# Kernel tuning notes

Hardware: AMD Instinct MI355X
Metric: run time of the kernel (lower is better)

## Reference

```python
import jax, jax.numpy as jnp
import numpy as np

DECAY = 0.8
EPS = 1e-05


def setup_inputs() -> dict:
    key = jax.random.key(0)
    k1, k2, k3 = jax.random.split(key, 3)
    x = jax.random.normal(k1, (8, 2048, 256), dtype=jnp.float32)
    embed = jax.random.normal(k2, (8192, 256), dtype=jnp.float32)
    cluster_size = jnp.zeros((8192,), dtype=jnp.float32)
    embed_avg = jax.random.normal(k3, (8192, 256), dtype=jnp.float32)
    return {"x": x, "embed": embed, "cluster_size": cluster_size, "embed_avg": embed_avg}


def reference(x, embed, cluster_size, embed_avg):
    codebook_size, dim = embed.shape
    shape = x.shape
    flatten = x.reshape(-1, dim)  # [N, d]

    dist = -(jnp.sum(flatten ** 2, axis=1, keepdims=True)
             - 2.0 * flatten @ embed.T
             + jnp.sum(embed ** 2, axis=1)[None, :])  # [N, C]
    embed_ind_flat = jnp.argmax(dist, axis=-1)  # [N]
    embed_ind = embed_ind_flat.reshape(shape[:-1])
    quantize = jnp.take(embed, embed_ind_flat, axis=0).reshape(shape)

    # EMA update (training branch). onehot matmuls expressed as segment sums.
    counts = jax.ops.segment_sum(jnp.ones_like(embed_ind_flat, dtype=x.dtype),
                                 embed_ind_flat, num_segments=codebook_size)  # [C]
    embed_sum = jax.ops.segment_sum(flatten, embed_ind_flat,
                                    num_segments=codebook_size)  # [C, d]
    cluster_size_new = cluster_size * DECAY + (1.0 - DECAY) * counts
    embed_avg_new = embed_avg * DECAY + (1.0 - DECAY) * embed_sum
    smoothed = (cluster_size_new + EPS) / (cluster_size_new.sum() + codebook_size * EPS)
    cs = smoothed * cluster_size_new.sum()
    embed_normalized = embed_avg_new / cs[:, None]

    return quantize, embed_ind, embed_normalized, cluster_size_new, embed_avg_new
```

## Files before the change

kernel.cpp:

```cpp
#include <hip/hip_runtime.h>
#include <hip/hip_bf16.h>

#define DECAY_F 0.8f
#define OMD_F   0.2f
#define EPS_F   1e-5f

#define NROWS 16384
#define CBOOK 8192
#define DIM   256
#define KSPLIT 768

#define WS_KEYS   0u
#define WS_ENORM  131072u
#define WS_COUNTS 163840u
#define WS_TOTAL  196608u
#define WS_XSPLIT 262144u
#define WS_ESPLIT 25428008u
#define WS_ESPLIT_OFF (262144u + 25165824u)
#define WS_NEED   (WS_ESPLIT_OFF + 12582912u)

#define O_QUANT 0
#define O_IND   4194304
#define O_NORM  4210688
#define O_CSN   6307840
#define O_AVG   6316032

typedef __attribute__((ext_vector_type(8))) short short8;
typedef __attribute__((ext_vector_type(4))) float f32x4;
typedef __attribute__((ext_vector_type(4))) unsigned short us4;

__device__ __forceinline__ unsigned int fkey(float f) {
    unsigned int b = __float_as_uint(f);
    return (b & 0x80000000u) ? ~b : (b | 0x80000000u);
}
__device__ __forceinline__ unsigned short f2bf(float f) {
    unsigned int u = __float_as_uint(f);
    unsigned int r = (u + 0x7FFFu + ((u >> 16) & 1u)) >> 16;
    return (unsigned short)r;
}
__device__ __forceinline__ float bf2f(unsigned short h) {
    return __uint_as_float(((unsigned int)h) << 16);
}

#define GLOAD_LDS16(g, l) \
    __builtin_amdgcn_global_load_lds((const __attribute__((address_space(1))) void*)(g), \
                                     (__attribute__((address_space(3))) void*)(l), 16, 0, 0)

__global__ __launch_bounds__(256) void enorm_kernel(const float* __restrict__ embed,
                                                    float* __restrict__ enorm) {
    int row  = (blockIdx.x * 256 + threadIdx.x) >> 6;
    int lane = threadIdx.x & 63;
    float4 v = *(const float4*)&embed[row * DIM + lane * 4];
    float s = v.x * v.x + v.y * v.y + v.z * v.z + v.w * v.w;
    for (int m = 32; m >= 1; m >>= 1) s += __shfl_xor(s, m, 64);
    if (lane == 0) enorm[row] = s;
}

__global__ __launch_bounds__(256) void init_avg_kernel(const float* __restrict__ embed_avg,
                                                       float* __restrict__ avg_out) {
    int i = blockIdx.x * 256 + threadIdx.x;
    float4 v = ((const float4*)embed_avg)[i];
    v.x *= DECAY_F; v.y *= DECAY_F; v.z *= DECAY_F; v.w *= DECAY_F;
    ((float4*)avg_out)[i] = v;
}

__global__ __launch_bounds__(256) void split_kernel(const float* __restrict__ src,
                                                    unsigned short* __restrict__ dst,
                                                    int pat) {
    int i = blockIdx.x * 256 + threadIdx.x;
    int e4  = i * 4;
    int row = e4 >> 8;
    int k   = e4 & 255;
    float4 v = ((const float4*)src)[i];
    us4 hi, lo;
    hi.x = f2bf(v.x); lo.x = f2bf(v.x - bf2f(hi.x));
    hi.y = f2bf(v.y); lo.y = f2bf(v.y - bf2f(hi.y));
    hi.z = f2bf(v.z); lo.z = f2bf(v.z - bf2f(hi.z));
    hi.w = f2bf(v.w); lo.w = f2bf(v.w - bf2f(hi.w));
    unsigned short* base = dst + (size_t)row * KSPLIT + k;
    *(us4*)(base + 0)   = hi;
    if (pat == 0) {
        *(us4*)(base + 256) = lo;
        *(us4*)(base + 512) = hi;
    } else {
        *(us4*)(base + 256) = hi;
        *(us4*)(base + 512) = lo;
    }
}

__global__ __launch_bounds__(256) void mfma_argmin_kernel(const unsigned short* __restrict__ A,
                                                          const unsigned short* __restrict__ B,
                                                          const float* __restrict__ enorm,
                                                          unsigned long long* __restrict__ keys) {
    __shared__ __align__(16) unsigned short Al[128 * 32];
    __shared__ __align__(16) unsigned short Bl[128 * 32];

    const int tid  = threadIdx.x;
    const int lane = tid & 63;
    const int wid  = tid >> 6;
    const int wr = wid >> 1, wc = wid & 1;
    const int mBase = blockIdx.y * 128;
    const int nBase = blockIdx.x * 128;

    const int lr = lane & 15;
    const int lk = (lane >> 4) * 8;

    f32x4 acc[4][4];
#pragma unroll
    for (int i = 0; i < 4; i++)
#pragma unroll
        for (int n = 0; n < 4; n++) acc[i][n] = (f32x4)0.f;

    const int r0  = tid >> 2;
    const int ck0 = (tid & 3) * 8;
    const unsigned short* srcA0 = A + (size_t)(mBase + r0) * KSPLIT + ck0;
    const unsigned short* srcA1 = srcA0 + (size_t)64 * KSPLIT;
    const unsigned short* srcB0 = B + (size_t)(nBase + r0) * KSPLIT + ck0;
    const unsigned short* srcB1 = srcB0 + (size_t)64 * KSPLIT;
    unsigned short* dstA0 = Al + tid * 8;
    unsigned short* dstA1 = Al + (tid + 256) * 8;
    unsigned short* dstB0 = Bl + tid * 8;
    unsigned short* dstB1 = Bl + (tid + 256) * 8;

    for (int kk = 0; kk < KSPLIT; kk += 32) {
        __syncthreads();
        GLOAD_LDS16(srcA0 + kk, dstA0);
        GLOAD_LDS16(srcA1 + kk, dstA1);
        GLOAD_LDS16(srcB0 + kk, dstB0);
        GLOAD_LDS16(srcB1 + kk, dstB1);
        __syncthreads();

        short8 af[4], bf[4];
#pragma unroll
        for (int i = 0; i < 4; i++)
            af[i] = *(const short8*)&Al[(wr * 64 + i * 16 + lr) * 32 + lk];
#pragma unroll
        for (int n = 0; n < 4; n++)
            bf[n] = *(const short8*)&Bl[(wc * 64 + n * 16 + lr) * 32 + lk];
#pragma unroll
        for (int i = 0; i < 4; i++)
#pragma unroll
            for (int n = 0; n < 4; n++)
                acc[i][n] = __builtin_amdgcn_mfma_f32_16x16x32_bf16(af[i], bf[n], acc[i][n], 0, 0, 0);
    }

    float en4[4];
    int   c4[4];
#pragma unroll
    for (int n = 0; n < 4; n++) {
        c4[n]  = nBase + wc * 64 + n * 16 + lr;
        en4[n] = enorm[c4[n]];
    }
#pragma unroll
    for (int i = 0; i < 4; i++) {
#pragma unroll
        for (int reg = 0; reg < 4; reg++) {
            float bs = 3.4e38f; int bc = 0;
#pragma unroll
            for (int n = 0; n < 4; n++) {
                float s = en4[n] - 2.f * acc[i][n][reg];
                if (s < bs || (s == bs && c4[n] < bc)) { bs = s; bc = c4[n]; }
            }
            unsigned long long key =
                ((unsigned long long)fkey(bs) << 32) | (unsigned int)bc;
#pragma unroll
            for (int m = 8; m >= 1; m >>= 1) {
                unsigned long long o = __shfl_xor(key, m, 64);
                if (o < key) key = o;
            }
            if (lr == 0)
                atomicMin(&keys[mBase + wr * 64 + i * 16 + (lane >> 4) * 4 + reg], key);
        }
    }
}

#define BM 64
#define BN 256
#define KB 16
#define NSPLIT 4

__global__ __launch_bounds__(256) void argmin_kernel(const float* __restrict__ x,
                                                     const float* __restrict__ embed,
                                                     const float* __restrict__ enorm,
                                                     unsigned long long* __restrict__ keys) {
    __shared__ float xs[KB][BM];
    __shared__ float es[KB][BN];

    const int tid = threadIdx.x;
    const int tx = tid & 31;
    const int ty = tid >> 5;
    const int rowBase = blockIdx.x * BM;
    const int cStart = blockIdx.y * (CBOOK / NSPLIT);

    float bestS[8];
    int   bestC[8];
#pragma unroll
    for (int i = 0; i < 8; i++) { bestS[i] = 3.4e38f; bestC[i] = 0; }

    float acc[8][8];

    for (int cb = 0; cb < CBOOK / NSPLIT; cb += BN) {
        const int cbase = cStart + cb;
#pragma unroll
        for (int i = 0; i < 8; i++)
#pragma unroll
            for (int j = 0; j < 8; j++) acc[i][j] = 0.f;

        for (int kk = 0; kk < DIM; kk += KB) {
            __syncthreads();
            {
                int r  = tid >> 2;
                int k4 = (tid & 3) * 4;
                float4 v = *(const float4*)&x[(rowBase + r) * DIM + kk + k4];
                xs[k4 + 0][r] = v.x; xs[k4 + 1][r] = v.y;
                xs[k4 + 2][r] = v.z; xs[k4 + 3][r] = v.w;
            }
            {
                const float4* src = (const float4*)&embed[(cbase + tid) * DIM + kk];
#pragma unroll
                for (int q = 0; q < 4; q++) {
                    float4 v = src[q];
                    es[q * 4 + 0][tid] = v.x; es[q * 4 + 1][tid] = v.y;
                    es[q * 4 + 2][tid] = v.z; es[q * 4 + 3][tid] = v.w;
                }
            }
            __syncthreads();
#pragma unroll
            for (int k = 0; k < KB; k++) {
                float xr[8], er[8];
                *(float4*)&xr[0] = *(const float4*)&xs[k][ty * 8];
                *(float4*)&xr[4] = *(const float4*)&xs[k][ty * 8 + 4];
                *(float4*)&er[0] = *(const float4*)&es[k][tx * 4];
                *(float4*)&er[4] = *(const float4*)&es[k][128 + tx * 4];
#pragma unroll
                for (int i = 0; i < 8; i++)
#pragma unroll
                    for (int j = 0; j < 8; j++)
                        acc[i][j] = fmaf(xr[i], er[j], acc[i][j]);
            }
        }
#pragma unroll
        for (int j = 0; j < 8; j++) {
            int c = cbase + ((j < 4) ? (tx * 4 + j) : (128 + tx * 4 + (j - 4)));
            float en = enorm[c];
#pragma unroll
            for (int i = 0; i < 8; i++) {
                float s = en - 2.f * acc[i][j];
                if (s < bestS[i]) { bestS[i] = s; bestC[i] = c; }
            }
        }
    }

#pragma unroll
    for (int i = 0; i < 8; i++) {
        unsigned long long key =
            ((unsigned long long)fkey(bestS[i]) << 32) | (unsigned int)bestC[i];
        for (int m = 16; m >= 1; m >>= 1) {
            unsigned long long o = __shfl_xor(key, m, 64);
            if (o < key) key = o;
        }
        if (tx == 0) atomicMin(&keys[rowBase + ty * 8 + i], key);
    }
}

__global__ __launch_bounds__(256) void scatter_kernel(const float* __restrict__ x,
                                                      const float* __restrict__ embed,
                                                      const unsigned long long* __restrict__ keys,
                                                      float* __restrict__ quant,
                                                      float* __restrict__ ind_out,
                                                      float* __restrict__ counts,
                                                      float* __restrict__ avg_out) {
    int i = blockIdx.x * 256 + threadIdx.x;
    int row = i >> 6;
    int c4  = (i & 63) * 4;
    int idx = (int)(keys[row] & 0xFFFFFFFFull);
    float4 e = *(const float4*)&embed[idx * DIM + c4];
    *(float4*)&quant[row * DIM + c4] = e;
    float4 xv = *(const float4*)&x[row * DIM + c4];
    atomicAdd(&avg_out[idx * DIM + c4 + 0], OMD_F * xv.x);
    atomicAdd(&avg_out[idx * DIM + c4 + 1], OMD_F * xv.y);
    atomicAdd(&avg_out[idx * DIM + c4 + 2], OMD_F * xv.z);
    atomicAdd(&avg_out[idx * DIM + c4 + 3], OMD_F * xv.w);
    if ((i & 63) == 0) {
        ind_out[row] = (float)idx;
        atomicAdd(&counts[idx], 1.0f);
    }
}

__global__ __launch_bounds__(256) void csn_kernel(const float* __restrict__ cluster_size,
                                                  const float* __restrict__ counts,
                                                  float* __restrict__ csn_out,
                                                  float* __restrict__ total) {
    int c = blockIdx.x * 256 + threadIdx.x;
    float v = DECAY_F * cluster_size[c] + OMD_F * counts[c];
    csn_out[c] = v;
    float s = v;
    for (int m = 32; m >= 1; m >>= 1) s += __shfl_xor(s, m, 64);
    __shared__ float ws4[4];
    if ((threadIdx.x & 63) == 0) ws4[threadIdx.x >> 6] = s;
    __syncthreads();
    if (threadIdx.x == 0) atomicAdd(total, ws4[0] + ws4[1] + ws4[2] + ws4[3]);
}

__global__ __launch_bounds__(256) void norm_kernel(const float* __restrict__ avg_new,
                                                   const float* __restrict__ csn,
                                                   const float* __restrict__ total,
                                                   float* __restrict__ out) {
    int i = blockIdx.x * 256 + threadIdx.x;
    int c = i >> 6;
    float tot = *total;
    float smoothed = (csn[c] + EPS_F) / (tot + (float)CBOOK * EPS_F);
    float cs = smoothed * tot;
    float4 v = ((const float4*)avg_new)[i];
    v.x = v.x / cs; v.y = v.y / cs; v.z = v.z / cs; v.w = v.w / cs;
    ((float4*)out)[i] = v;
}

extern "C" void kernel_launch(void* const* d_in, const int* in_sizes, int n_in,
                              void* d_out, int out_size, void* d_ws, size_t ws_size,
                              hipStream_t stream) {
    const float* x            = (const float*)d_in[0];
    const float* embed        = (const float*)d_in[1];
    const float* cluster_size = (const float*)d_in[2];
    const float* embed_avg    = (const float*)d_in[3];
    float* out = (float*)d_out;
    char*  ws  = (char*)d_ws;

    unsigned long long* keys = (unsigned long long*)(ws + WS_KEYS);
    float* enorm  = (float*)(ws + WS_ENORM);
    float* counts = (float*)(ws + WS_COUNTS);
    float* total  = (float*)(ws + WS_TOTAL);

    hipMemsetAsync(ws + WS_KEYS, 0xFF, NROWS * 8, stream);
    hipMemsetAsync(ws + WS_COUNTS, 0, CBOOK * 4 + 4, stream);

    enorm_kernel<<<CBOOK / 4, 256, 0, stream>>>(embed, enorm);
    init_avg_kernel<<<(CBOOK * DIM / 4) / 256, 256, 0, stream>>>(embed_avg, out + O_AVG);

    if (ws_size >= (size_t)WS_NEED) {
        unsigned short* xsplit = (unsigned short*)(ws + WS_XSPLIT);
        unsigned short* esplit = (unsigned short*)(ws + WS_ESPLIT_OFF);
        split_kernel<<<(NROWS * DIM / 4) / 256, 256, 0, stream>>>(x, xsplit, 0);
        split_kernel<<<(CBOOK * DIM / 4) / 256, 256, 0, stream>>>(embed, esplit, 1);
        dim3 grid(CBOOK / 128, NROWS / 128);
        mfma_argmin_kernel<<<grid, 256, 0, stream>>>(xsplit, esplit, enorm, keys);
    } else {
        dim3 grid(NROWS / BM, NSPLIT);
        argmin_kernel<<<grid, 256, 0, stream>>>(x, embed, enorm, keys);
    }

    scatter_kernel<<<(NROWS * DIM / 4) / 256, 256, 0, stream>>>(
        x, embed, keys, out + O_QUANT, out + O_IND, counts, out + O_AVG);

    csn_kernel<<<CBOOK / 256, 256, 0, stream>>>(cluster_size, counts, out + O_CSN, total);

    norm_kernel<<<(CBOOK * DIM / 4) / 256, 256, 0, stream>>>(
        out + O_AVG, out + O_CSN, total, out + O_NORM);
}
```

Baseline: 454.4 us.

## Double-buffer LDS with swizzle in MFMA argmin and fuse enorm into esplit

The MFMA distance kernel now double-buffers its LDS tiles, so the global-to-LDS loads for the next K slice are issued before the current slice's MFMAs, with one barrier per iteration instead of two. It also XOR-swizzles the 16-byte chunk layout in LDS to cut bank conflicts on fragment reads, and adds an occupancy hint to launch bounds. Separately, the codebook norm computation is folded into the embed split kernel, which removes one launch and one read of the codebook. The trade-off is twice the LDS per block, which may limit occupancy.

```diff
diff --git a/kernel.cpp b/kernel.cpp
--- a/kernel.cpp
+++ b/kernel.cpp
@@ -15,7 +15,6 @@
 #define WS_COUNTS 163840u
 #define WS_TOTAL  196608u
 #define WS_XSPLIT 262144u
-#define WS_ESPLIT 25428008u
 #define WS_ESPLIT_OFF (262144u + 25165824u)
 #define WS_NEED   (WS_ESPLIT_OFF + 12582912u)
 
@@ -45,16 +44,6 @@
 #define GLOAD_LDS16(g, l) \
     __builtin_amdgcn_global_load_lds((const __attribute__((address_space(1))) void*)(g), \
                                      (__attribute__((address_space(3))) void*)(l), 16, 0, 0)
-
-__global__ __launch_bounds__(256) void enorm_kernel(const float* __restrict__ embed,
-                                                    float* __restrict__ enorm) {
-    int row  = (blockIdx.x * 256 + threadIdx.x) >> 6;
-    int lane = threadIdx.x & 63;
-    float4 v = *(const float4*)&embed[row * DIM + lane * 4];
-    float s = v.x * v.x + v.y * v.y + v.z * v.z + v.w * v.w;
-    for (int m = 32; m >= 1; m >>= 1) s += __shfl_xor(s, m, 64);
-    if (lane == 0) enorm[row] = s;
-}
 
 __global__ __launch_bounds__(256) void init_avg_kernel(const float* __restrict__ embed_avg,
                                                        float* __restrict__ avg_out) {
@@ -64,9 +53,8 @@
     ((float4*)avg_out)[i] = v;
 }
 
-__global__ __launch_bounds__(256) void split_kernel(const float* __restrict__ src,
-                                                    unsigned short* __restrict__ dst,
-                                                    int pat) {
+__global__ __launch_bounds__(256) void xsplit_kernel(const float* __restrict__ src,
+                                                     unsigned short* __restrict__ dst) {
     int i = blockIdx.x * 256 + threadIdx.x;
     int e4  = i * 4;
     int row = e4 >> 8;
@@ -79,21 +67,36 @@
     hi.w = f2bf(v.w); lo.w = f2bf(v.w - bf2f(hi.w));
     unsigned short* base = dst + (size_t)row * KSPLIT + k;
     *(us4*)(base + 0)   = hi;
-    if (pat == 0) {
-        *(us4*)(base + 256) = lo;
-        *(us4*)(base + 512) = hi;
-    } else {
-        *(us4*)(base + 256) = hi;
-        *(us4*)(base + 512) = lo;
-    }
-}
-
-__global__ __launch_bounds__(256) void mfma_argmin_kernel(const unsigned short* __restrict__ A,
-                                                          const unsigned short* __restrict__ B,
-                                                          const float* __restrict__ enorm,
-                                                          unsigned long long* __restrict__ keys) {
-    __shared__ __align__(16) unsigned short Al[128 * 32];
-    __shared__ __align__(16) unsigned short Bl[128 * 32];
+    *(us4*)(base + 256) = lo;
+    *(us4*)(base + 512) = hi;
+}
+
+__global__ __launch_bounds__(256) void esplit_kernel(const float* __restrict__ embed,
+                                                     unsigned short* __restrict__ dst,
+                                                     float* __restrict__ enorm) {
+    int row  = (blockIdx.x * 256 + threadIdx.x) >> 6;
+    int lane = threadIdx.x & 63;
+    float4 v = *(const float4*)&embed[row * DIM + lane * 4];
+    float s = v.x * v.x + v.y * v.y + v.z * v.z + v.w * v.w;
+    for (int m = 32; m >= 1; m >>= 1) s += __shfl_xor(s, m, 64);
+    if (lane == 0) enorm[row] = s;
+    us4 hi, lo;
+    hi.x = f2bf(v.x); lo.x = f2bf(v.x - bf2f(hi.x));
+    hi.y = f2bf(v.y); lo.y = f2bf(v.y - bf2f(hi.y));
+    hi.z = f2bf(v.z); lo.z = f2bf(v.z - bf2f(hi.z));
+    hi.w = f2bf(v.w); lo.w = f2bf(v.w - bf2f(hi.w));
+    unsigned short* base = dst + (size_t)row * KSPLIT + lane * 4;
+    *(us4*)(base + 0)   = hi;
+    *(us4*)(base + 256) = hi;
+    *(us4*)(base + 512) = lo;
+}
+
+__global__ __launch_bounds__(256, 4) void mfma_argmin_kernel(const unsigned short* __restrict__ A,
+                                                             const unsigned short* __restrict__ B,
+                                                             const float* __restrict__ enorm,
+                                                             unsigned long long* __restrict__ keys) {
+    __shared__ __align__(16) unsigned short Al[2][128 * 32];
+    __shared__ __align__(16) unsigned short Bl[2][128 * 32];
 
     const int tid  = threadIdx.x;
     const int lane = tid & 63;
@@ -103,7 +106,7 @@
     const int nBase = blockIdx.x * 128;
 
     const int lr = lane & 15;
-    const int lk = (lane >> 4) * 8;
+    const int hk = lane >> 4;
 
     f32x4 acc[4][4];
 #pragma unroll
@@ -111,38 +114,50 @@
 #pragma unroll
         for (int n = 0; n < 4; n++) acc[i][n] = (f32x4)0.f;
 
-    const int r0  = tid >> 2;
-    const int ck0 = (tid & 3) * 8;
-    const unsigned short* srcA0 = A + (size_t)(mBase + r0) * KSPLIT + ck0;
-    const unsigned short* srcA1 = srcA0 + (size_t)64 * KSPLIT;
-    const unsigned short* srcB0 = B + (size_t)(nBase + r0) * KSPLIT + ck0;
-    const unsigned short* srcB1 = srcB0 + (size_t)64 * KSPLIT;
-    unsigned short* dstA0 = Al + tid * 8;
-    unsigned short* dstA1 = Al + (tid + 256) * 8;
-    unsigned short* dstB0 = Bl + tid * 8;
-    unsigned short* dstB1 = Bl + (tid + 256) * 8;
-
-    for (int kk = 0; kk < KSPLIT; kk += 32) {
+    const int r0 = tid >> 2;
+    const int ck = (((tid & 3) ^ ((r0 >> 1) & 3)) << 3);
+    const unsigned short* gA0 = A + (size_t)(mBase + r0) * KSPLIT + ck;
+    const unsigned short* gA1 = gA0 + (size_t)64 * KSPLIT;
+    const unsigned short* gB0 = B + (size_t)(nBase + r0) * KSPLIT + ck;
+    const unsigned short* gB1 = gB0 + (size_t)64 * KSPLIT;
+
+#define STAGE(b, kk) do { \
+    GLOAD_LDS16(gA0 + (kk), &Al[b][tid * 8]); \
+    GLOAD_LDS16(gA1 + (kk), &Al[b][(tid + 256) * 8]); \
+    GLOAD_LDS16(gB0 + (kk), &Bl[b][tid * 8]); \
+    GLOAD_LDS16(gB1 + (kk), &Bl[b][(tid + 256) * 8]); \
+} while (0)
+
+    const int co = ((hk ^ ((lr >> 1) & 3)) << 3);
+    int aoff[4], boff[4];
+#pragma unroll
+    for (int i = 0; i < 4; i++) {
+        aoff[i] = (wr * 64 + i * 16 + lr) * 32 + co;
+        boff[i] = (wc * 64 + i * 16 + lr) * 32 + co;
+    }
+
+    STAGE(0, 0);
+    __syncthreads();
+
+#pragma unroll 2
+    for (int t = 0; t < 24; ++t) {
+        const int cur = t & 1;
+        if (t < 23) STAGE(cur ^ 1, (t + 1) * 32);
+
+        short8 af[4], bf4[4];
+#pragma unroll
+        for (int i = 0; i < 4; i++) af[i]  = *(const short8*)&Al[cur][aoff[i]];
+#pragma unroll
+        for (int n = 0; n < 4; n++) bf4[n] = *(const short8*)&Bl[cur][boff[n]];
+#pragma unroll
+        for (int i = 0; i < 4; i++)
+#pragma unroll
+            for (int n = 0; n < 4; n++)
+                acc[i][n] = __builtin_amdgcn_mfma_f32_16x16x32_bf16(af[i], bf4[n], acc[i][n], 0, 0, 0);
+
         __syncthreads();
-        GLOAD_LDS16(srcA0 + kk, dstA0);
-        GLOAD_LDS16(srcA1 + kk, dstA1);
-        GLOAD_LDS16(srcB0 + kk, dstB0);
-        GLOAD_LDS16(srcB1 + kk, dstB1);
-        __syncthreads();
-
-        short8 af[4], bf[4];
-#pragma unroll
-        for (int i = 0; i < 4; i++)
-            af[i] = *(const short8*)&Al[(wr * 64 + i * 16 + lr) * 32 + lk];
-#pragma unroll
-        for (int n = 0; n < 4; n++)
-            bf[n] = *(const short8*)&Bl[(wc * 64 + n * 16 + lr) * 32 + lk];
-#pragma unroll
-        for (int i = 0; i < 4; i++)
-#pragma unroll
-            for (int n = 0; n < 4; n++)
-                acc[i][n] = __builtin_amdgcn_mfma_f32_16x16x32_bf16(af[i], bf[n], acc[i][n], 0, 0, 0);
-    }
+    }
+#undef STAGE
 
     float en4[4];
     int   c4[4];
@@ -169,7 +184,7 @@
                 if (o < key) key = o;
             }
             if (lr == 0)
-                atomicMin(&keys[mBase + wr * 64 + i * 16 + (lane >> 4) * 4 + reg], key);
+                atomicMin(&keys[mBase + wr * 64 + i * 16 + hk * 4 + reg], key);
         }
     }
 }
@@ -334,17 +349,17 @@
     hipMemsetAsync(ws + WS_KEYS, 0xFF, NROWS * 8, stream);
     hipMemsetAsync(ws + WS_COUNTS, 0, CBOOK * 4 + 4, stream);
 
-    enorm_kernel<<<CBOOK / 4, 256, 0, stream>>>(embed, enorm);
     init_avg_kernel<<<(CBOOK * DIM / 4) / 256, 256, 0, stream>>>(embed_avg, out + O_AVG);
 
     if (ws_size >= (size_t)WS_NEED) {
         unsigned short* xsplit = (unsigned short*)(ws + WS_XSPLIT);
         unsigned short* esplit = (unsigned short*)(ws + WS_ESPLIT_OFF);
-        split_kernel<<<(NROWS * DIM / 4) / 256, 256, 0, stream>>>(x, xsplit, 0);
-        split_kernel<<<(CBOOK * DIM / 4) / 256, 256, 0, stream>>>(embed, esplit, 1);
+        xsplit_kernel<<<(NROWS * DIM / 4) / 256, 256, 0, stream>>>(x, xsplit);
+        esplit_kernel<<<CBOOK / 4, 256, 0, stream>>>(embed, esplit, enorm);
         dim3 grid(CBOOK / 128, NROWS / 128);
         mfma_argmin_kernel<<<grid, 256, 0, stream>>>(xsplit, esplit, enorm, keys);
     } else {
+        esplit_kernel<<<CBOOK / 4, 256, 0, stream>>>(embed, (unsigned short*)(ws + WS_XSPLIT), enorm);
         dim3 grid(NROWS / BM, NSPLIT);
         argmin_kernel<<<grid, 256, 0, stream>>>(x, embed, enorm, keys);
     }
```

New measurement: 404.8 us. 10.9% less time.
